# Kernel tuning notes

Measured on AMD Instinct MI355X. Metric: run time of the kernel, lower is better.

Reference implementation:

```python
import jax, jax.numpy as jnp
import numpy as np

B, F, E, H = 4096, 26, 64, 1000000
D = F * E  # 1664

def setup_inputs() -> dict:
    key = jax.random.key(0)
    ks = jax.random.split(key, 12)
    s = 0.02  # init scale
    return {
        "ids": jax.random.randint(ks[0], (B, F), 0, H),
        "emb": jax.random.normal(ks[1], (H, E), jnp.float32) * s,
        "cross_w": jax.random.normal(ks[2], (3, D), jnp.float32) * s,
        "cross_b": jnp.zeros((3, D), jnp.float32),
        "w1": jax.random.normal(ks[3], (D, 1024), jnp.float32) * s,
        "b1": jnp.zeros((1024,), jnp.float32),
        "w2": jax.random.normal(ks[4], (1024, 512), jnp.float32) * s,
        "b2": jnp.zeros((512,), jnp.float32),
        "w3": jax.random.normal(ks[5], (512, 256), jnp.float32) * s,
        "b3": jnp.zeros((256,), jnp.float32),
        "out_w": jax.random.normal(ks[6], (D + 256, 1), jnp.float32) * s,
        "out_b": jnp.zeros((), jnp.float32),
    }

def reference(ids, emb, cross_w, cross_b, w1, b1, w2, b2, w3, b3, out_w, out_b):
    # Embedding lookup + field-wise concat -> x0: [B, D]
    x0 = emb[ids].reshape(ids.shape[0], -1)
    # Cross net. Original materializes [B,D,D] outer product x0 * x^T then
    # giving the same math with O(B*D) memory.
    x = x0
    for i in range(cross_w.shape[0]):
        s = x @ cross_w[i]                 # [B] per-example scalar
        x = x0 * s[:, None] + cross_b[i] + x
    # Deep tower on x0
    h = jax.nn.relu(x0 @ w1 + b1)
    h = jax.nn.relu(h @ w2 + b2)
    h = jax.nn.relu(h @ w3 + b3)
    # Output head
    logit = jnp.concatenate([x, h], axis=1) @ out_w + out_b  # [B, 1]
    return jax.nn.sigmoid(logit)
```

## Files before the change

kernel.cpp:

```cpp
#include <hip/hip_runtime.h>
#include <hip/hip_bf16.h>

#define B_  4096
#define F_  26
#define E_  64
#define D_  1664
#define N1_ 1024
#define N2_ 512
#define N3_ 256

typedef __attribute__((ext_vector_type(8))) __bf16 bf16x8;
typedef __attribute__((ext_vector_type(4))) float  f32x4;

__device__ __forceinline__ unsigned short f2b(float x) {
    __hip_bfloat16 h = __float2bfloat16(x);
    return __builtin_bit_cast(unsigned short, h);
}
__device__ __forceinline__ float b2f(unsigned short u) {
    return __uint_as_float(((unsigned)u) << 16);
}

__device__ __forceinline__ void async_load16(const void* g, void* l) {
    __builtin_amdgcn_global_load_lds(
        (const __attribute__((address_space(1))) void*)g,
        (__attribute__((address_space(3))) void*)l,
        16, 0, 0);
}

__device__ __forceinline__ f32x4 mfma16(bf16x8 a, bf16x8 b, f32x4 c) {
    return __builtin_amdgcn_mfma_f32_16x16x32_bf16(a, b, c, 0, 0, 0);
}

__global__ __launch_bounds__(256) void gather_kernel(
        const int* __restrict__ ids, const float* __restrict__ emb,
        unsigned short* __restrict__ x0b)
{
    const int t  = blockIdx.x * 256 + threadIdx.x;
    const int e4 = t * 4;
    if (e4 >= B_ * D_) return;
    const int b = e4 / D_;
    const int d = e4 - b * D_;
    const int f = d >> 6;
    const int e = d & 63;
    const int id = ids[b * F_ + f];
    const float4 v = *(const float4*)(emb + (size_t)id * E_ + e);
    ushort4 o;
    o.x = f2b(v.x); o.y = f2b(v.y); o.z = f2b(v.z); o.w = f2b(v.w);
    *(ushort4*)(x0b + e4) = o;
}

__global__ __launch_bounds__(256) void transpose_cast_kernel(
        const float* __restrict__ in, unsigned short* __restrict__ out,
        int K, int N)
{
    __shared__ float tile[32][33];
    const int n0 = blockIdx.x * 32, k0 = blockIdx.y * 32;
    const int tc = threadIdx.x & 31, tr = threadIdx.x >> 5;
    #pragma unroll
    for (int p = 0; p < 4; p++)
        tile[tr + p * 8][tc] = in[(size_t)(k0 + tr + p * 8) * N + n0 + tc];
    __syncthreads();
    #pragma unroll
    for (int p = 0; p < 4; p++) {
        const int n = tr + p * 8;
        out[(size_t)(n0 + n) * K + k0 + tc] = f2b(tile[tc][n]);
    }
}

__global__ __launch_bounds__(256) void cross_head_kernel(
        const unsigned short* __restrict__ x0b,
        const float* __restrict__ cw, const float* __restrict__ cb,
        const float* __restrict__ out_w, float* __restrict__ partial)
{
    __shared__ float red[4];
    const int b = blockIdx.x;
    const int t = threadIdx.x;
    const int lane = t & 63, w = t >> 6;
    const unsigned short* xr = x0b + (size_t)b * D_;

    float x0r[7], xv[7];
    #pragma unroll
    for (int j = 0; j < 7; j++) {
        const int d = t + j * 256;
        const float v = (d < D_) ? b2f(xr[d]) : 0.f;
        x0r[j] = v; xv[j] = v;
    }
    for (int i = 0; i < 3; i++) {
        float s = 0.f;
        #pragma unroll
        for (int j = 0; j < 7; j++) {
            const int d = t + j * 256;
            if (d < D_) s += xv[j] * cw[i * D_ + d];
        }
        #pragma unroll
        for (int off = 32; off > 0; off >>= 1) s += __shfl_down(s, off, 64);
        __syncthreads();
        if (lane == 0) red[w] = s;
        __syncthreads();
        const float st = red[0] + red[1] + red[2] + red[3];
        #pragma unroll
        for (int j = 0; j < 7; j++) {
            const int d = t + j * 256;
            if (d < D_) xv[j] = x0r[j] * st + cb[i * D_ + d] + xv[j];
        }
    }
    float s = 0.f;
    #pragma unroll
    for (int j = 0; j < 7; j++) {
        const int d = t + j * 256;
        if (d < D_) s += xv[j] * out_w[d];
    }
    #pragma unroll
    for (int off = 32; off > 0; off >>= 1) s += __shfl_down(s, off, 64);
    __syncthreads();
    if (lane == 0) red[w] = s;
    __syncthreads();
    if (t == 0) partial[b] = red[0] + red[1] + red[2] + red[3];
}

template<int BM, int BN>
__global__ __launch_bounds__(256) void gemm_bias_relu(
        const unsigned short* __restrict__ A,
        const unsigned short* __restrict__ Bt,
        const float* __restrict__ bias,
        unsigned short* __restrict__ C,
        int M, int N, int K)
{
    constexpr int BK = 32;
    constexpr int WM = BM / 2, WN = BN / 2;
    constexpr int TI = WM / 16, TJ = WN / 16;
    constexpr int CA = BM / 64, CB = BN / 64;

    __shared__ unsigned short sA[BM * BK];
    __shared__ unsigned short sB[BN * BK];

    const int t    = threadIdx.x;
    const int lane = t & 63;
    const int w    = t >> 6;
    const int m0   = blockIdx.y * BM;
    const int n0   = blockIdx.x * BN;
    const int wm   = (w >> 1) * WM;
    const int wn   = (w & 1) * WN;

    const int srow = lane >> 2;
    const int scol = (lane & 3) * 8;

    f32x4 acc[TI][TJ] = {};

    for (int k0 = 0; k0 < K; k0 += BK) {
        #pragma unroll
        for (int c = 0; c < CA; c++) {
            const int chunk = w * CA + c;
            const unsigned short* g =
                A + (size_t)(m0 + chunk * 16 + srow) * K + k0 + scol;
            async_load16(g, &sA[chunk * 512]);
        }
        #pragma unroll
        for (int c = 0; c < CB; c++) {
            const int chunk = w * CB + c;
            const unsigned short* g =
                Bt + (size_t)(n0 + chunk * 16 + srow) * K + k0 + scol;
            async_load16(g, &sB[chunk * 512]);
        }
        __syncthreads();

        bf16x8 af[TI], bf[TJ];
        #pragma unroll
        for (int i = 0; i < TI; i++)
            af[i] = *(const bf16x8*)&sA[(wm + i * 16 + (lane & 15)) * BK + (lane >> 4) * 8];
        #pragma unroll
        for (int j = 0; j < TJ; j++)
            bf[j] = *(const bf16x8*)&sB[(wn + j * 16 + (lane & 15)) * BK + (lane >> 4) * 8];
        #pragma unroll
        for (int i = 0; i < TI; i++)
            #pragma unroll
            for (int j = 0; j < TJ; j++)
                acc[i][j] = mfma16(af[i], bf[j], acc[i][j]);
        __syncthreads();
    }

    #pragma unroll
    for (int i = 0; i < TI; i++) {
        const int r0 = m0 + wm + i * 16 + (lane >> 4) * 4;
        #pragma unroll
        for (int j = 0; j < TJ; j++) {
            const int col = n0 + wn + j * 16 + (lane & 15);
            const float bv = bias[col];
            #pragma unroll
            for (int r = 0; r < 4; r++) {
                float v = acc[i][j][r] + bv;
                v = fmaxf(v, 0.f);
                C[(size_t)(r0 + r) * N + col] = f2b(v);
            }
        }
    }
}

__global__ __launch_bounds__(256) void head_kernel(
        const float* __restrict__ partial, const unsigned short* __restrict__ h3,
        const float* __restrict__ out_w, const float* __restrict__ out_b,
        float* __restrict__ out)
{
    const int gw   = (blockIdx.x * 256 + threadIdx.x) >> 6;
    const int lane = threadIdx.x & 63;
    if (gw >= B_) return;
    float s = 0.f;
    #pragma unroll
    for (int q = 0; q < 4; q++) {
        const int j = lane + q * 64;
        s += b2f(h3[(size_t)gw * N3_ + j]) * out_w[D_ + j];
    }
    #pragma unroll
    for (int off = 32; off > 0; off >>= 1) s += __shfl_down(s, off, 64);
    if (lane == 0) {
        const float logit = partial[gw] + s + out_b[0];
        out[gw] = 1.f / (1.f + expf(-logit));
    }
}

extern "C" void kernel_launch(void* const* d_in, const int* in_sizes, int n_in,
                              void* d_out, int out_size, void* d_ws, size_t ws_size,
                              hipStream_t stream)
{
    (void)in_sizes; (void)n_in; (void)out_size; (void)ws_size;
    const int*   ids     = (const int*)  d_in[0];
    const float* emb     = (const float*)d_in[1];
    const float* cross_w = (const float*)d_in[2];
    const float* cross_b = (const float*)d_in[3];
    const float* w1      = (const float*)d_in[4];
    const float* b1      = (const float*)d_in[5];
    const float* w2      = (const float*)d_in[6];
    const float* b2      = (const float*)d_in[7];
    const float* w3      = (const float*)d_in[8];
    const float* b3      = (const float*)d_in[9];
    const float* out_w   = (const float*)d_in[10];
    const float* out_b   = (const float*)d_in[11];
    float* out = (float*)d_out;

    char* p = (char*)d_ws;
    auto alloc = [&](size_t bytes) {
        char* r = p; p += (bytes + 255) & ~(size_t)255; return r;
    };
    unsigned short* x0b = (unsigned short*)alloc((size_t)B_ * D_ * 2);
    unsigned short* w1t = (unsigned short*)alloc((size_t)D_ * N1_ * 2);
    unsigned short* w2t = (unsigned short*)alloc((size_t)N1_ * N2_ * 2);
    unsigned short* w3t = (unsigned short*)alloc((size_t)N2_ * N3_ * 2);
    unsigned short* h1  = (unsigned short*)alloc((size_t)B_ * N1_ * 2);
    unsigned short* h2  = (unsigned short*)alloc((size_t)B_ * N2_ * 2);
    unsigned short* h3  = (unsigned short*)alloc((size_t)B_ * N3_ * 2);
    float* partial      = (float*)alloc((size_t)B_ * 4);

    gather_kernel<<<(B_ * D_ / 4) / 256, 256, 0, stream>>>(ids, emb, x0b);
    transpose_cast_kernel<<<dim3(N1_ / 32, D_  / 32), 256, 0, stream>>>(w1, w1t, D_,  N1_);
    transpose_cast_kernel<<<dim3(N2_ / 32, N1_ / 32), 256, 0, stream>>>(w2, w2t, N1_, N2_);
    transpose_cast_kernel<<<dim3(N3_ / 32, N2_ / 32), 256, 0, stream>>>(w3, w3t, N2_, N3_);
    cross_head_kernel<<<B_, 256, 0, stream>>>(x0b, cross_w, cross_b, out_w, partial);

    gemm_bias_relu<128, 128><<<dim3(N1_ / 128, B_ / 128), 256, 0, stream>>>(
        x0b, w1t, b1, h1, B_, N1_, D_);
    gemm_bias_relu<128, 64><<<dim3(N2_ / 64, B_ / 128), 256, 0, stream>>>(
        h1, w2t, b2, h2, B_, N2_, N1_);
    gemm_bias_relu<64, 64><<<dim3(N3_ / 64, B_ / 64), 256, 0, stream>>>(
        h2, w3t, b3, h3, B_, N3_, N2_);

    head_kernel<<<B_ / 4, 256, 0, stream>>>(partial, h3, out_w, out_b, out);
}
```

Before: 426.4 us.

## Fuse embedding gather into cross kernel, deepen GEMM K-step, remap blocks per XCD

```diff
diff --git a/kernel.cpp b/kernel.cpp
--- a/kernel.cpp
+++ b/kernel.cpp
@@ -31,58 +31,31 @@
     return __builtin_amdgcn_mfma_f32_16x16x32_bf16(a, b, c, 0, 0, 0);
 }
 
-__global__ __launch_bounds__(256) void gather_kernel(
+__global__ __launch_bounds__(256) void gather_cross_kernel(
         const int* __restrict__ ids, const float* __restrict__ emb,
-        unsigned short* __restrict__ x0b)
-{
-    const int t  = blockIdx.x * 256 + threadIdx.x;
-    const int e4 = t * 4;
-    if (e4 >= B_ * D_) return;
-    const int b = e4 / D_;
-    const int d = e4 - b * D_;
-    const int f = d >> 6;
-    const int e = d & 63;
-    const int id = ids[b * F_ + f];
-    const float4 v = *(const float4*)(emb + (size_t)id * E_ + e);
-    ushort4 o;
-    o.x = f2b(v.x); o.y = f2b(v.y); o.z = f2b(v.z); o.w = f2b(v.w);
-    *(ushort4*)(x0b + e4) = o;
-}
-
-__global__ __launch_bounds__(256) void transpose_cast_kernel(
-        const float* __restrict__ in, unsigned short* __restrict__ out,
-        int K, int N)
-{
-    __shared__ float tile[32][33];
-    const int n0 = blockIdx.x * 32, k0 = blockIdx.y * 32;
-    const int tc = threadIdx.x & 31, tr = threadIdx.x >> 5;
-    #pragma unroll
-    for (int p = 0; p < 4; p++)
-        tile[tr + p * 8][tc] = in[(size_t)(k0 + tr + p * 8) * N + n0 + tc];
-    __syncthreads();
-    #pragma unroll
-    for (int p = 0; p < 4; p++) {
-        const int n = tr + p * 8;
-        out[(size_t)(n0 + n) * K + k0 + tc] = f2b(tile[tc][n]);
-    }
-}
-
-__global__ __launch_bounds__(256) void cross_head_kernel(
-        const unsigned short* __restrict__ x0b,
         const float* __restrict__ cw, const float* __restrict__ cb,
-        const float* __restrict__ out_w, float* __restrict__ partial)
-{
+        const float* __restrict__ out_w,
+        unsigned short* __restrict__ x0b, float* __restrict__ partial)
+{
+    __shared__ int   sid[F_];
     __shared__ float red[4];
     const int b = blockIdx.x;
     const int t = threadIdx.x;
     const int lane = t & 63, w = t >> 6;
-    const unsigned short* xr = x0b + (size_t)b * D_;
+
+    if (t < F_) sid[t] = ids[b * F_ + t];
+    __syncthreads();
 
     float x0r[7], xv[7];
     #pragma unroll
     for (int j = 0; j < 7; j++) {
         const int d = t + j * 256;
-        const float v = (d < D_) ? b2f(xr[d]) : 0.f;
+        float v = 0.f;
+        if (d < D_) {
+            const int f = d >> 6;
+            v = emb[(size_t)sid[f] * E_ + (d & 63)];
+            x0b[(size_t)b * D_ + d] = f2b(v);
+        }
         x0r[j] = v; xv[j] = v;
     }
     for (int i = 0; i < 3; i++) {
@@ -116,6 +89,24 @@
     if (lane == 0) red[w] = s;
     __syncthreads();
     if (t == 0) partial[b] = red[0] + red[1] + red[2] + red[3];
+}
+
+__global__ __launch_bounds__(256) void transpose_cast_kernel(
+        const float* __restrict__ in, unsigned short* __restrict__ out,
+        int K, int N)
+{
+    __shared__ float tile[32][33];
+    const int n0 = blockIdx.x * 32, k0 = blockIdx.y * 32;
+    const int tc = threadIdx.x & 31, tr = threadIdx.x >> 5;
+    #pragma unroll
+    for (int p = 0; p < 4; p++)
+        tile[tr + p * 8][tc] = in[(size_t)(k0 + tr + p * 8) * N + n0 + tc];
+    __syncthreads();
+    #pragma unroll
+    for (int p = 0; p < 4; p++) {
+        const int n = tr + p * 8;
+        out[(size_t)(n0 + n) * K + k0 + tc] = f2b(tile[tc][n]);
+    }
 }
 
 template<int BM, int BN>
@@ -126,19 +117,26 @@
         unsigned short* __restrict__ C,
         int M, int N, int K)
 {
-    constexpr int BK = 32;
     constexpr int WM = BM / 2, WN = BN / 2;
     constexpr int TI = WM / 16, TJ = WN / 16;
-    constexpr int CA = BM / 64, CB = BN / 64;
-
-    __shared__ unsigned short sA[BM * BK];
-    __shared__ unsigned short sB[BN * BK];
+    constexpr int nA = BM / 16, nB = BN / 16, nAB = nA + nB;
+    constexpr int TOTC = 2 * nAB;
+
+    __shared__ unsigned short sA[2 * BM * 32];
+    __shared__ unsigned short sB[2 * BN * 32];
 
     const int t    = threadIdx.x;
     const int lane = t & 63;
     const int w    = t >> 6;
-    const int m0   = blockIdx.y * BM;
-    const int n0   = blockIdx.x * BN;
+
+    const int i    = blockIdx.y * gridDim.x + blockIdx.x;
+    const int xcd  = i & 7;
+    const int s    = i >> 3;
+    const int ypg  = gridDim.y >> 3;
+    const int ty   = xcd * ypg + s / gridDim.x;
+    const int tx   = s - (s / gridDim.x) * gridDim.x;
+    const int m0   = ty * BM;
+    const int n0   = tx * BN;
     const int wm   = (w >> 1) * WM;
     const int wn   = (w & 1) * WN;
 
@@ -147,48 +145,55 @@
 
     f32x4 acc[TI][TJ] = {};
 
-    for (int k0 = 0; k0 < K; k0 += BK) {
-        #pragma unroll
-        for (int c = 0; c < CA; c++) {
-            const int chunk = w * CA + c;
-            const unsigned short* g =
-                A + (size_t)(m0 + chunk * 16 + srow) * K + k0 + scol;
-            async_load16(g, &sA[chunk * 512]);
-        }
-        #pragma unroll
-        for (int c = 0; c < CB; c++) {
-            const int chunk = w * CB + c;
-            const unsigned short* g =
-                Bt + (size_t)(n0 + chunk * 16 + srow) * K + k0 + scol;
-            async_load16(g, &sB[chunk * 512]);
-        }
-        __syncthreads();
-
-        bf16x8 af[TI], bf[TJ];
-        #pragma unroll
-        for (int i = 0; i < TI; i++)
-            af[i] = *(const bf16x8*)&sA[(wm + i * 16 + (lane & 15)) * BK + (lane >> 4) * 8];
-        #pragma unroll
-        for (int j = 0; j < TJ; j++)
-            bf[j] = *(const bf16x8*)&sB[(wn + j * 16 + (lane & 15)) * BK + (lane >> 4) * 8];
-        #pragma unroll
-        for (int i = 0; i < TI; i++)
+    for (int k0 = 0; k0 < K; k0 += 64) {
+        #pragma unroll
+        for (int c0 = 0; c0 < TOTC; c0 += 4) {
+            const int c = c0 + w;
+            const int u = c / nAB;
+            const int r = c - u * nAB;
+            if (r < nA) {
+                const unsigned short* g =
+                    A + (size_t)(m0 + r * 16 + srow) * K + k0 + u * 32 + scol;
+                async_load16(g, &sA[u * BM * 32 + r * 512]);
+            } else {
+                const int rb = r - nA;
+                const unsigned short* g =
+                    Bt + (size_t)(n0 + rb * 16 + srow) * K + k0 + u * 32 + scol;
+                async_load16(g, &sB[u * BN * 32 + rb * 512]);
+            }
+        }
+        __syncthreads();
+
+        #pragma unroll
+        for (int u = 0; u < 2; u++) {
+            bf16x8 af[TI], bf[TJ];
+            #pragma unroll
+            for (int ii = 0; ii < TI; ii++)
+                af[ii] = *(const bf16x8*)
+                    &sA[u * BM * 32 + (wm + ii * 16 + (lane & 15)) * 32 + (lane >> 4) * 8];
             #pragma unroll
             for (int j = 0; j < TJ; j++)
-                acc[i][j] = mfma16(af[i], bf[j], acc[i][j]);
-        __syncthreads();
-    }
-
-    #pragma unroll
-    for (int i = 0; i < TI; i++) {
-        const int r0 = m0 + wm + i * 16 + (lane >> 4) * 4;
+                bf[j] = *(const bf16x8*)
+                    &sB[u * BN * 32 + (wn + j * 16 + (lane & 15)) * 32 + (lane >> 4) * 8];
+            #pragma unroll
+            for (int ii = 0; ii < TI; ii++)
+                #pragma unroll
+                for (int j = 0; j < TJ; j++)
+                    acc[ii][j] = mfma16(af[ii], bf[j], acc[ii][j]);
+        }
+        __syncthreads();
+    }
+
+    #pragma unroll
+    for (int ii = 0; ii < TI; ii++) {
+        const int r0 = m0 + wm + ii * 16 + (lane >> 4) * 4;
         #pragma unroll
         for (int j = 0; j < TJ; j++) {
             const int col = n0 + wn + j * 16 + (lane & 15);
             const float bv = bias[col];
             #pragma unroll
             for (int r = 0; r < 4; r++) {
-                float v = acc[i][j][r] + bv;
+                float v = acc[ii][j][r] + bv;
                 v = fmaxf(v, 0.f);
                 C[(size_t)(r0 + r) * N + col] = f2b(v);
             }
@@ -250,17 +255,17 @@
     unsigned short* h3  = (unsigned short*)alloc((size_t)B_ * N3_ * 2);
     float* partial      = (float*)alloc((size_t)B_ * 4);
 
-    gather_kernel<<<(B_ * D_ / 4) / 256, 256, 0, stream>>>(ids, emb, x0b);
+    gather_cross_kernel<<<B_, 256, 0, stream>>>(
+        ids, emb, cross_w, cross_b, out_w, x0b, partial);
     transpose_cast_kernel<<<dim3(N1_ / 32, D_  / 32), 256, 0, stream>>>(w1, w1t, D_,  N1_);
     transpose_cast_kernel<<<dim3(N2_ / 32, N1_ / 32), 256, 0, stream>>>(w2, w2t, N1_, N2_);
     transpose_cast_kernel<<<dim3(N3_ / 32, N2_ / 32), 256, 0, stream>>>(w3, w3t, N2_, N3_);
-    cross_head_kernel<<<B_, 256, 0, stream>>>(x0b, cross_w, cross_b, out_w, partial);
-
-    gemm_bias_relu<128, 128><<<dim3(N1_ / 128, B_ / 128), 256, 0, stream>>>(
+
+    gemm_bias_relu<128, 64><<<dim3(N1_ / 64, B_ / 128), 256, 0, stream>>>(
         x0b, w1t, b1, h1, B_, N1_, D_);
-    gemm_bias_relu<128, 64><<<dim3(N2_ / 64, B_ / 128), 256, 0, stream>>>(
+    gemm_bias_relu<64, 64><<<dim3(N2_ / 64, B_ / 64), 256, 0, stream>>>(
         h1, w2t, b2, h2, B_, N2_, N1_);
-    gemm_bias_relu<64, 64><<<dim3(N3_ / 64, B_ / 64), 256, 0, stream>>>(
+    gemm_bias_relu<64, 32><<<dim3(N3_ / 32, B_ / 64), 256, 0, stream>>>(
         h2, w3t, b3, h3, B_, N3_, N2_);
 
     head_kernel<<<B_ / 4, 256, 0, stream>>>(partial, h3, out_w, out_b, out);
```

After: 395.4 us. 7.3% less time.
